# Kernel tuning notes

Hardware: AMD Instinct MI355X
Metric: run time of the kernel (lower is better)

## Reference

```python
import jax, jax.numpy as jnp
import numpy as np

T, B, H = 2048, 8, 16
KF, VF, KS, VS = 32, 64, 128, 64


def _l2norm(x, eps=1e-6):
    return x / jnp.sqrt(jnp.sum(x * x, axis=-1, keepdims=True) + eps)


def setup_inputs() -> dict:
    key = jax.random.key(0)
    ks = jax.random.split(key, 12)
    # k/q are L2-normalized externally (per E88/E90 kernel contract)
    k_fast = _l2norm(jax.random.normal(ks[0], (T, B, H, KF), jnp.float32))
    q_fast = _l2norm(jax.random.normal(ks[1], (T, B, H, KF), jnp.float32))
    v_fast = jax.random.normal(ks[2], (T, B, H, VF), jnp.float32)
    k_slow = _l2norm(jax.random.normal(ks[3], (T, B, H, KS), jnp.float32))
    q_slow = _l2norm(jax.random.normal(ks[4], (T, B, H, KS), jnp.float32))
    v_slow = jax.random.normal(ks[5], (T, B, H, VS), jnp.float32)
    # decay factors in (0.85, 1.0): typical Mamba2-style per-head scalar decay
    decay_fast = 0.85 + 0.15 * jax.random.uniform(ks[6], (T, B, H), jnp.float32)
    decay_slow = 0.85 + 0.15 * jax.random.uniform(ks[7], (T, B, H), jnp.float32)
    slow_gate = jax.random.uniform(ks[8], (T, B, H), jnp.float32)
    mix_fast = jax.random.uniform(ks[9], (T, B, H), jnp.float32)
    mix_slow = jax.random.uniform(ks[10], (T, B, H), jnp.float32)
    S_fast0 = jnp.zeros((B, H, KF, VF), jnp.float32)
    S_slow0 = jnp.zeros((B, H, KS, VS), jnp.float32)
    return dict(k_fast=k_fast, v_fast=v_fast, q_fast=q_fast, decay_fast=decay_fast,
                k_slow=k_slow, v_slow=v_slow, q_slow=q_slow, decay_slow=decay_slow,
                slow_gate=slow_gate, mix_fast=mix_fast, mix_slow=mix_slow,
                S_fast0=S_fast0, S_slow0=S_slow0, n_heads=H)


def _e90_scan(k_fast, v_fast, q_fast, decay_fast,
              k_slow, v_slow, q_slow, decay_slow,
              slow_gate, mix_fast, mix_slow, S_fast0, S_slow0):
    def step(carry, x):
        S_f, S_s = carry  # [B,H,KF,VF], [B,H,KS,VS]
        kf, vf, qf, df, ksl, vsl, qsl, dsl, g, mf, ms = x
        # fast state: updated every timestep (decay + rank-1 outer product)
        S_f = df[..., None, None] * S_f + kf[..., :, None] * vf[..., None, :]
        # slow state: gated soft update
        S_s_new = dsl[..., None, None] * S_s + ksl[..., :, None] * vsl[..., None, :]
        g_ = g[..., None, None]
        S_s = g_ * S_s_new + (1.0 - g_) * S_s
        out_f = jnp.einsum('bhk,bhkv->bhv', qf, S_f)
        out_s = jnp.einsum('bhk,bhkv->bhv', qsl, S_s)
        out = mf[..., None] * out_f + ms[..., None] * out_s
        return (S_f, S_s), out

    xs = (k_fast, v_fast, q_fast, decay_fast,
          k_slow, v_slow, q_slow, decay_slow,
          slow_gate, mix_fast, mix_slow)
    (S_f_final, S_s_final), output = jax.lax.scan(step, (S_fast0, S_slow0), xs)
    return S_f_final, S_s_final, output  # output: [T,B,H,VF]


def reference(k_fast, v_fast, q_fast, decay_fast, k_slow, v_slow, q_slow,
              decay_slow, slow_gate, mix_fast, mix_slow, S_fast0, S_slow0, n_heads):
    return _e90_scan(k_fast, v_fast, q_fast, decay_fast,
                     k_slow, v_slow, q_slow, decay_slow,
                     slow_gate, mix_fast, mix_slow, S_fast0, S_slow0)
```

## Files before the change

### kernel.cpp

```cpp
#include <hip/hip_runtime.h>

#define T_STEPS 2048
#define BH      128
#define KS_     128
#define VS_     64
#define KF_     32
#define VF_     64
#define LCH     32
#define NC      (T_STEPS / LCH)
#define NTHR    512

typedef __attribute__((ext_vector_type(8))) short short8;
typedef __attribute__((ext_vector_type(16))) float f32x16;

#define MFMA32(a,b,c) __builtin_amdgcn_mfma_f32_32x32x16_bf16((a),(b),(c),0,0,0)
#define CROW(r,hi) (((r)&3) + 8*((r)>>2) + 4*(hi))

__device__ __forceinline__ unsigned short f2b(float x) {
    union { float f; unsigned u; } v; v.f = x;
    unsigned r = v.u + 0x7FFFu + ((v.u >> 16) & 1u);
    return (unsigned short)(r >> 16);
}

__device__ __forceinline__ short8 ld8(const unsigned short* p) {
    return *(const short8*)p;
}

__global__ __launch_bounds__(NTHR, 2)
void e90_mfma(const float* __restrict__ k_fast,  const float* __restrict__ v_fast,
              const float* __restrict__ q_fast,  const float* __restrict__ decay_fast,
              const float* __restrict__ k_slow,  const float* __restrict__ v_slow,
              const float* __restrict__ q_slow,  const float* __restrict__ decay_slow,
              const float* __restrict__ slow_gate, const float* __restrict__ mix_fast,
              const float* __restrict__ mix_slow, const float* __restrict__ S_fast0,
              const float* __restrict__ S_slow0, float* __restrict__ dout)
{
    __shared__ __align__(16) unsigned short Qs [LCH][136];
    __shared__ __align__(16) unsigned short Ksl[LCH][136];
    __shared__ __align__(16) unsigned short Sbs[LCH][136];
    __shared__ __align__(16) unsigned short Psl[LCH][40];
    __shared__ __align__(16) unsigned short Qfl[LCH][40];
    __shared__ __align__(16) unsigned short Kfl[LCH][40];
    __shared__ __align__(16) unsigned short Sbfl[LCH][40];
    __shared__ __align__(16) unsigned short Pfl[LCH][40];
    __shared__ __align__(16) unsigned short VTs[2][LCH][40];
    __shared__ __align__(16) unsigned short VTf[2][LCH][40];

    const int tid  = threadIdx.x;
    const int bid  = blockIdx.x;
    const int xcd  = bid & 7;
    const int jj   = bid >> 3;
    const int p    = xcd * 16 + (jj >> 1);
    const int v0   = (jj & 1) * 32;
    const int lane = tid & 63;
    const int wid  = tid >> 6;
    const int l31  = lane & 31;
    const int hi   = lane >> 5;
    const int s_   = tid >> 4;
    const int j0_  = (tid & 15) * 2;
    const int k0_  = (tid & 15) * 8;

    float* out_y = dout + BH*KF_*VF_ + BH*KS_*VS_;

    f32x16 Sst, oacc;
#pragma unroll
    for (int r = 0; r < 16; ++r) { Sst[r] = 0.0f; oacc[r] = 0.0f; }
    if (wid < 4) {
#pragma unroll
        for (int r = 0; r < 16; ++r)
            Sst[r] = S_slow0[((size_t)p*KS_ + 32*wid + CROW(r,hi))*VS_ + v0 + l31];
#pragma unroll
        for (int r = 0; r < 16; ++r) Sbs[l31][32*wid + CROW(r,hi)] = f2b(Sst[r]);
    } else if (wid == 4) {
#pragma unroll
        for (int r = 0; r < 16; ++r)
            Sst[r] = S_fast0[((size_t)p*KF_ + CROW(r,hi))*VF_ + v0 + l31];
#pragma unroll
        for (int r = 0; r < 16; ++r) Sbfl[l31][CROW(r,hi)] = f2b(Sst[r]);
    }

    float4 pKs0, pKs1, pQs0, pQs1;
    float2 pVs, pVf, pKf, pQf;
    float pL0 = 0.f, pL1 = 0.f, pL2 = 0.f;

#define LOADCHUNK(CIDX) do {                                                   \
    int tc_ = (CIDX); if (tc_ > NC-1) tc_ = NC-1;                              \
    const int tb_ = tc_ * LCH;                                                 \
    const float* bk_ = k_slow + ((size_t)(tb_+s_)*BH + p)*KS_ + k0_;           \
    pKs0 = *(const float4*)bk_;  pKs1 = *(const float4*)(bk_+4);               \
    const float* bq_ = q_slow + ((size_t)(tb_+s_)*BH + p)*KS_ + k0_;           \
    pQs0 = *(const float4*)bq_;  pQs1 = *(const float4*)(bq_+4);               \
    pVs = *(const float2*)(v_slow + ((size_t)(tb_+s_)*BH + p)*VS_ + v0 + j0_); \
    pVf = *(const float2*)(v_fast + ((size_t)(tb_+s_)*BH + p)*VF_ + v0 + j0_); \
    pKf = *(const float2*)(k_fast + ((size_t)(tb_+s_)*BH + p)*KF_ + j0_);      \
    pQf = *(const float2*)(q_fast + ((size_t)(tb_+s_)*BH + p)*KF_ + j0_);      \
    const size_t so_ = (size_t)(tb_ + l31)*BH + p;                             \
    pL0 = (hi ? decay_fast : decay_slow)[so_];                                 \
    pL1 = (hi ? mix_fast   : slow_gate )[so_];                                 \
    pL2 = hi ? 0.0f : mix_slow[so_];                                           \
    } while (0)

    LOADCHUNK(0);

    float bls = 1.f, blf = 1.f, ib = 1.f, ibf = 1.f, qsc = 0.f, qfc = 0.f, g_s = 0.f;

    for (int c = 0; c < NC; ++c) {
        const int cb = c & 1;
        if (c > 0) {
            if (wid < 4) {
#pragma unroll
                for (int r = 0; r < 16; ++r) Sbs[l31][32*wid + CROW(r,hi)] = f2b(Sst[r]);
            } else if (wid == 4) {
#pragma unroll
                for (int r = 0; r < 16; ++r) Sbfl[l31][CROW(r,hi)] = f2b(Sst[r]);
            } else if (wid == 7) {
                const int pb = cb ^ 1;
                f32x16 o2;
#pragma unroll
                for (int r = 0; r < 16; ++r) o2[r] = 0.0f;
                const unsigned short* ar = &Psl[l31][0];
                const unsigned short* br = &VTs[pb][l31][0];
                oacc = MFMA32(ld8(ar + 8*hi),      ld8(br + 8*hi),      oacc);
                oacc = MFMA32(ld8(ar + 16 + 8*hi), ld8(br + 16 + 8*hi), oacc);
                const unsigned short* af = &Pfl[l31][0];
                const unsigned short* bf = &VTf[pb][l31][0];
                o2 = MFMA32(ld8(af + 8*hi),      ld8(bf + 8*hi),      o2);
                o2 = MFMA32(ld8(af + 16 + 8*hi), ld8(bf + 16 + 8*hi), o2);
#pragma unroll
                for (int r = 0; r < 16; ++r) {
                    int tr = CROW(r,hi);
                    out_y[((size_t)((c-1)*LCH + tr)*BH + p)*VF_ + v0 + l31] = oacc[r] + o2[r];
                }
            }
        }
        {
            float a = hi ? pL0 : __builtin_fmaf(pL1, pL0, 1.0f - pL1);
            float b = a;
#pragma unroll
            for (int d = 1; d < 32; d <<= 1) {
                float y = __shfl_up(b, d, 32);
                if (l31 >= d) b *= y;
            }
            float bs_s = __shfl(b, s_);
            float bf_s = __shfl(b, 32 + s_);
            bls = __shfl(b, 31);
            blf = __shfl(b, 63);
            g_s = __shfl(pL1, s_);
            float mf_s = __shfl(pL1, 32 + s_);
            float ms_s = __shfl(pL2, s_);
            ib  = 1.0f / bs_s;
            ibf = 1.0f / bf_s;
            qsc = ms_s * bs_s;
            qfc = mf_s * bf_s;
        }
        {
            float kv[8] = {pKs0.x,pKs0.y,pKs0.z,pKs0.w,pKs1.x,pKs1.y,pKs1.z,pKs1.w};
            float qv[8] = {pQs0.x,pQs0.y,pQs0.z,pQs0.w,pQs1.x,pQs1.y,pQs1.z,pQs1.w};
            unsigned short kb[8], qb[8];
#pragma unroll
            for (int e = 0; e < 8; ++e) { kb[e] = f2b(kv[e]*ib); qb[e] = f2b(qv[e]*qsc); }
            uint4 kw, qw;
            kw.x = kb[0] | ((unsigned)kb[1]<<16); kw.y = kb[2] | ((unsigned)kb[3]<<16);
            kw.z = kb[4] | ((unsigned)kb[5]<<16); kw.w = kb[6] | ((unsigned)kb[7]<<16);
            qw.x = qb[0] | ((unsigned)qb[1]<<16); qw.y = qb[2] | ((unsigned)qb[3]<<16);
            qw.z = qb[4] | ((unsigned)qb[5]<<16); qw.w = qb[6] | ((unsigned)qb[7]<<16);
            *(uint4*)&Ksl[s_][k0_] = kw;
            *(uint4*)&Qs [s_][k0_] = qw;

            float vt0 = g_s*pVs.x, vt1 = g_s*pVs.y;
            VTs[cb][j0_  ][s_] = f2b(vt0);
            VTs[cb][j0_+1][s_] = f2b(vt1);
            VTf[cb][j0_  ][s_] = f2b(pVf.x);
            VTf[cb][j0_+1][s_] = f2b(pVf.y);
            unsigned kfp = f2b(pKf.x*ibf) | ((unsigned)f2b(pKf.y*ibf) << 16);
            *(unsigned*)&Kfl[s_][j0_] = kfp;
            unsigned qfp = f2b(pQf.x*qfc) | ((unsigned)f2b(pQf.y*qfc) << 16);
            *(unsigned*)&Qfl[s_][j0_] = qfp;
        }
        __syncthreads();

        LOADCHUNK(c + 1);

        if (wid < 4) {
            short8 a1, a2;
#pragma unroll
            for (int e = 0; e < 8; ++e) {
                a1[e] = (short)Ksl[8*hi + e][32*wid + l31];
                a2[e] = (short)Ksl[16 + 8*hi + e][32*wid + l31];
            }
            const unsigned short* br = &VTs[cb][l31][0];
            Sst = MFMA32(a1, ld8(br + 8*hi),      Sst);
            Sst = MFMA32(a2, ld8(br + 16 + 8*hi), Sst);
#pragma unroll
            for (int r = 0; r < 16; ++r) Sst[r] *= bls;
        } else if (wid == 4) {
            short8 a1, a2;
#pragma unroll
            for (int e = 0; e < 8; ++e) {
                a1[e] = (short)Kfl[8*hi + e][l31];
                a2[e] = (short)Kfl[16 + 8*hi + e][l31];
            }
            const unsigned short* br = &VTf[cb][l31][0];
            Sst = MFMA32(a1, ld8(br + 8*hi),      Sst);
            Sst = MFMA32(a2, ld8(br + 16 + 8*hi), Sst);
#pragma unroll
            for (int r = 0; r < 16; ++r) Sst[r] *= blf;
        } else if (wid == 5) {
            f32x16 p1, p2;
#pragma unroll
            for (int r = 0; r < 16; ++r) { p1[r] = 0.0f; p2[r] = 0.0f; }
            const unsigned short* ar = &Qs [l31][0];
            const unsigned short* br = &Ksl[l31][0];
            const int kb = 8*hi;
#pragma unroll
            for (int st = 0; st < 8; st += 2) {
                p1 = MFMA32(ld8(ar + kb + 16*st),     ld8(br + kb + 16*st),     p1);
                p2 = MFMA32(ld8(ar + kb + 16*(st+1)), ld8(br + kb + 16*(st+1)), p2);
            }
#pragma unroll
            for (int r = 0; r < 16; ++r) {
                int tr = CROW(r,hi);
                Psl[tr][l31] = f2b(tr >= l31 ? p1[r] + p2[r] : 0.0f);
            }
        } else if (wid == 6) {
            f32x16 p1;
#pragma unroll
            for (int r = 0; r < 16; ++r) p1[r] = 0.0f;
            const unsigned short* ar = &Qfl[l31][0];
            const unsigned short* br = &Kfl[l31][0];
            p1 = MFMA32(ld8(ar + 8*hi),      ld8(br + 8*hi),      p1);
            p1 = MFMA32(ld8(ar + 16 + 8*hi), ld8(br + 16 + 8*hi), p1);
#pragma unroll
            for (int r = 0; r < 16; ++r) {
                int tr = CROW(r,hi);
                Pfl[tr][l31] = f2b(tr >= l31 ? p1[r] : 0.0f);
            }
        } else {
            f32x16 o1, o2;
#pragma unroll
            for (int r = 0; r < 16; ++r) { o1[r] = 0.0f; o2[r] = 0.0f; }
            const unsigned short* ar = &Qs [l31][0];
            const unsigned short* br = &Sbs[l31][0];
            const int kb = 8*hi;
#pragma unroll
            for (int st = 0; st < 8; st += 2) {
                o1 = MFMA32(ld8(ar + kb + 16*st),     ld8(br + kb + 16*st),     o1);
                o2 = MFMA32(ld8(ar + kb + 16*(st+1)), ld8(br + kb + 16*(st+1)), o2);
            }
            const unsigned short* af = &Qfl [l31][0];
            const unsigned short* bf = &Sbfl[l31][0];
            o1 = MFMA32(ld8(af + 8*hi),      ld8(bf + 8*hi),      o1);
            o2 = MFMA32(ld8(af + 16 + 8*hi), ld8(bf + 16 + 8*hi), o2);
#pragma unroll
            for (int r = 0; r < 16; ++r) oacc[r] = o1[r] + o2[r];
        }
        __syncthreads();
    }

    if (wid == 7) {
        const int pb = (NC - 1) & 1;
        f32x16 o2;
#pragma unroll
        for (int r = 0; r < 16; ++r) o2[r] = 0.0f;
        const unsigned short* ar = &Psl[l31][0];
        const unsigned short* br = &VTs[pb][l31][0];
        oacc = MFMA32(ld8(ar + 8*hi),      ld8(br + 8*hi),      oacc);
        oacc = MFMA32(ld8(ar + 16 + 8*hi), ld8(br + 16 + 8*hi), oacc);
        const unsigned short* af = &Pfl[l31][0];
        const unsigned short* bf = &VTf[pb][l31][0];
        o2 = MFMA32(ld8(af + 8*hi),      ld8(bf + 8*hi),      o2);
        o2 = MFMA32(ld8(af + 16 + 8*hi), ld8(bf + 16 + 8*hi), o2);
#pragma unroll
        for (int r = 0; r < 16; ++r) {
            int tr = CROW(r,hi);
            out_y[((size_t)((NC-1)*LCH + tr)*BH + p)*VF_ + v0 + l31] = oacc[r] + o2[r];
        }
    }

    if (wid < 4) {
#pragma unroll
        for (int r = 0; r < 16; ++r)
            dout[BH*KF_*VF_ + ((size_t)p*KS_ + 32*wid + CROW(r,hi))*VS_ + v0 + l31] = Sst[r];
    } else if (wid == 4) {
#pragma unroll
        for (int r = 0; r < 16; ++r)
            dout[((size_t)p*KF_ + CROW(r,hi))*VF_ + v0 + l31] = Sst[r];
    }
#undef LOADCHUNK
}

extern "C" void kernel_launch(void* const* d_in, const int* in_sizes, int n_in,
                              void* d_out, int out_size, void* d_ws, size_t ws_size,
                              hipStream_t stream)
{
    const float* k_fast     = (const float*)d_in[0];
    const float* v_fast     = (const float*)d_in[1];
    const float* q_fast     = (const float*)d_in[2];
    const float* decay_fast = (const float*)d_in[3];
    const float* k_slow     = (const float*)d_in[4];
    const float* v_slow     = (const float*)d_in[5];
    const float* q_slow     = (const float*)d_in[6];
    const float* decay_slow = (const float*)d_in[7];
    const float* slow_gate  = (const float*)d_in[8];
    const float* mix_fast   = (const float*)d_in[9];
    const float* mix_slow   = (const float*)d_in[10];
    const float* S_fast0    = (const float*)d_in[11];
    const float* S_slow0    = (const float*)d_in[12];
    float* dout = (float*)d_out;

    e90_mfma<<<dim3(256), dim3(NTHR), 0, stream>>>(
        k_fast, v_fast, q_fast, decay_fast,
        k_slow, v_slow, q_slow, decay_slow,
        slow_gate, mix_fast, mix_slow, S_fast0, S_slow0, dout);
}
```

Baseline: 205.4 us.

## Double-buffer chunk staging to drop a barrier per chunk and use packed bf16 converts

Shared-memory staging buffers are now double-buffered (triple for the V transposes). The next chunk's K/Q/V staging, decay scan and state writeback happen after the current chunk's MFMA work, so each chunk needs one __syncthreads instead of two. The scalar loads are prefetched two chunks ahead. The manual bf16 rounding used for K/Q packing is replaced with the v_cvt_pk_bf16_f32 instruction. This costs more LDS, which could reduce occupancy, and the staging work now sits serially after the compute inside the same barrier interval.

Measured after the change: 186.9 us (median of 2 runs). 9.0% less time.

```diff
diff --git a/kernel.cpp b/kernel.cpp
--- a/kernel.cpp
+++ b/kernel.cpp
@@ -21,7 +21,11 @@
     unsigned r = v.u + 0x7FFFu + ((v.u >> 16) & 1u);
     return (unsigned short)(r >> 16);
 }
-
+__device__ __forceinline__ unsigned cvtpk(float lo, float hi_) {
+    unsigned r;
+    asm("v_cvt_pk_bf16_f32 %0, %1, %2" : "=v"(r) : "v"(lo), "v"(hi_));
+    return r;
+}
 __device__ __forceinline__ short8 ld8(const unsigned short* p) {
     return *(const short8*)p;
 }
@@ -35,16 +39,16 @@
               const float* __restrict__ mix_slow, const float* __restrict__ S_fast0,
               const float* __restrict__ S_slow0, float* __restrict__ dout)
 {
-    __shared__ __align__(16) unsigned short Qs [LCH][136];
-    __shared__ __align__(16) unsigned short Ksl[LCH][136];
-    __shared__ __align__(16) unsigned short Sbs[LCH][136];
-    __shared__ __align__(16) unsigned short Psl[LCH][40];
-    __shared__ __align__(16) unsigned short Qfl[LCH][40];
-    __shared__ __align__(16) unsigned short Kfl[LCH][40];
-    __shared__ __align__(16) unsigned short Sbfl[LCH][40];
-    __shared__ __align__(16) unsigned short Pfl[LCH][40];
-    __shared__ __align__(16) unsigned short VTs[2][LCH][40];
-    __shared__ __align__(16) unsigned short VTf[2][LCH][40];
+    __shared__ __align__(16) unsigned short Qs  [2][LCH][136];
+    __shared__ __align__(16) unsigned short Ksl [2][LCH][136];
+    __shared__ __align__(16) unsigned short Sbs [2][LCH][136];
+    __shared__ __align__(16) unsigned short Psl [2][LCH][40];
+    __shared__ __align__(16) unsigned short Pfl [2][LCH][40];
+    __shared__ __align__(16) unsigned short Qfl [2][LCH][40];
+    __shared__ __align__(16) unsigned short Kfl [2][LCH][40];
+    __shared__ __align__(16) unsigned short Sbfl[2][LCH][40];
+    __shared__ __align__(16) unsigned short VTs [3][LCH][40];
+    __shared__ __align__(16) unsigned short VTf [3][LCH][40];
 
     const int tid  = threadIdx.x;
     const int bid  = blockIdx.x;
@@ -70,20 +74,21 @@
         for (int r = 0; r < 16; ++r)
             Sst[r] = S_slow0[((size_t)p*KS_ + 32*wid + CROW(r,hi))*VS_ + v0 + l31];
 #pragma unroll
-        for (int r = 0; r < 16; ++r) Sbs[l31][32*wid + CROW(r,hi)] = f2b(Sst[r]);
+        for (int r = 0; r < 16; ++r) Sbs[0][l31][32*wid + CROW(r,hi)] = f2b(Sst[r]);
     } else if (wid == 4) {
 #pragma unroll
         for (int r = 0; r < 16; ++r)
             Sst[r] = S_fast0[((size_t)p*KF_ + CROW(r,hi))*VF_ + v0 + l31];
 #pragma unroll
-        for (int r = 0; r < 16; ++r) Sbfl[l31][CROW(r,hi)] = f2b(Sst[r]);
+        for (int r = 0; r < 16; ++r) Sbfl[0][l31][CROW(r,hi)] = f2b(Sst[r]);
     }
 
     float4 pKs0, pKs1, pQs0, pQs1;
     float2 pVs, pVf, pKf, pQf;
     float pL0 = 0.f, pL1 = 0.f, pL2 = 0.f;
-
-#define LOADCHUNK(CIDX) do {                                                   \
+    float bls = 1.f, blf = 1.f, ib = 1.f, ibf = 1.f, qsc = 0.f, qfc = 0.f, g_s = 0.f;
+
+#define LOADVEC(CIDX) do {                                                     \
     int tc_ = (CIDX); if (tc_ > NC-1) tc_ = NC-1;                              \
     const int tb_ = tc_ * LCH;                                                 \
     const float* bk_ = k_slow + ((size_t)(tb_+s_)*BH + p)*KS_ + k0_;           \
@@ -94,101 +99,97 @@
     pVf = *(const float2*)(v_fast + ((size_t)(tb_+s_)*BH + p)*VF_ + v0 + j0_); \
     pKf = *(const float2*)(k_fast + ((size_t)(tb_+s_)*BH + p)*KF_ + j0_);      \
     pQf = *(const float2*)(q_fast + ((size_t)(tb_+s_)*BH + p)*KF_ + j0_);      \
-    const size_t so_ = (size_t)(tb_ + l31)*BH + p;                             \
+    } while (0)
+
+#define LOADSCL(CIDX) do {                                                     \
+    int tc_ = (CIDX); if (tc_ > NC-1) tc_ = NC-1;                              \
+    const size_t so_ = (size_t)(tc_*LCH + l31)*BH + p;                         \
     pL0 = (hi ? decay_fast : decay_slow)[so_];                                 \
     pL1 = (hi ? mix_fast   : slow_gate )[so_];                                 \
     pL2 = hi ? 0.0f : mix_slow[so_];                                           \
     } while (0)
 
-    LOADCHUNK(0);
-
-    float bls = 1.f, blf = 1.f, ib = 1.f, ibf = 1.f, qsc = 0.f, qfc = 0.f, g_s = 0.f;
+#define SCAN() do {                                                            \
+    float a_ = hi ? pL0 : __builtin_fmaf(pL1, pL0, 1.0f - pL1);                \
+    float b_ = a_;                                                             \
+    _Pragma("unroll")                                                          \
+    for (int d = 1; d < 32; d <<= 1) {                                         \
+        float y_ = __shfl_up(b_, d, 32);                                       \
+        if (l31 >= d) b_ *= y_;                                                \
+    }                                                                          \
+    float bs_s = __shfl(b_, s_);                                               \
+    float bf_s = __shfl(b_, 32 + s_);                                          \
+    bls = __shfl(b_, 31);                                                      \
+    blf = __shfl(b_, 63);                                                      \
+    g_s = __shfl(pL1, s_);                                                     \
+    float mf_s = __shfl(pL1, 32 + s_);                                         \
+    float ms_s = __shfl(pL2, s_);                                              \
+    ib  = 1.0f / bs_s;                                                         \
+    ibf = 1.0f / bf_s;                                                         \
+    qsc = ms_s * bs_s;                                                         \
+    qfc = mf_s * bf_s;                                                         \
+    } while (0)
+
+#define STAGE(J2, J3) do {                                                     \
+    uint4 kw, qw;                                                              \
+    kw.x = cvtpk(pKs0.x*ib, pKs0.y*ib);  kw.y = cvtpk(pKs0.z*ib, pKs0.w*ib);   \
+    kw.z = cvtpk(pKs1.x*ib, pKs1.y*ib);  kw.w = cvtpk(pKs1.z*ib, pKs1.w*ib);   \
+    qw.x = cvtpk(pQs0.x*qsc, pQs0.y*qsc); qw.y = cvtpk(pQs0.z*qsc, pQs0.w*qsc);\
+    qw.z = cvtpk(pQs1.x*qsc, pQs1.y*qsc); qw.w = cvtpk(pQs1.z*qsc, pQs1.w*qsc);\
+    *(uint4*)&Ksl[J2][s_][k0_] = kw;                                           \
+    *(uint4*)&Qs [J2][s_][k0_] = qw;                                           \
+    float vt0 = g_s*pVs.x, vt1 = g_s*pVs.y;                                    \
+    VTs[J3][j0_  ][s_] = f2b(vt0);                                             \
+    VTs[J3][j0_+1][s_] = f2b(vt1);                                             \
+    VTf[J3][j0_  ][s_] = f2b(pVf.x);                                           \
+    VTf[J3][j0_+1][s_] = f2b(pVf.y);                                           \
+    unsigned kfp = cvtpk(pKf.x*ibf, pKf.y*ibf);                                \
+    *(unsigned*)&Kfl[J2][s_][j0_] = kfp;                                       \
+    unsigned qfp = cvtpk(pQf.x*qfc, pQf.y*qfc);                                \
+    *(unsigned*)&Qfl[J2][s_][j0_] = qfp;                                       \
+    } while (0)
+
+#define YSTORE(CP) do {                                                        \
+    const int p2_ = (CP) & 1, p3_ = (CP) % 3;                                  \
+    f32x16 o2;                                                                 \
+    _Pragma("unroll")                                                          \
+    for (int r = 0; r < 16; ++r) o2[r] = 0.0f;                                 \
+    const unsigned short* ar = &Psl[p2_][l31][0];                              \
+    const unsigned short* br = &VTs[p3_][l31][0];                              \
+    oacc = MFMA32(ld8(ar + 8*hi),      ld8(br + 8*hi),      oacc);             \
+    oacc = MFMA32(ld8(ar + 16 + 8*hi), ld8(br + 16 + 8*hi), oacc);             \
+    const unsigned short* af = &Pfl[p2_][l31][0];                              \
+    const unsigned short* bf = &VTf[p3_][l31][0];                              \
+    o2 = MFMA32(ld8(af + 8*hi),      ld8(bf + 8*hi),      o2);                 \
+    o2 = MFMA32(ld8(af + 16 + 8*hi), ld8(bf + 16 + 8*hi), o2);                 \
+    _Pragma("unroll")                                                          \
+    for (int r = 0; r < 16; ++r) {                                             \
+        int tr = CROW(r,hi);                                                   \
+        out_y[((size_t)((CP)*LCH + tr)*BH + p)*VF_ + v0 + l31] = oacc[r] + o2[r]; \
+    }                                                                          \
+    } while (0)
+
+    LOADVEC(0);
+    LOADSCL(0);
+    SCAN();
+    LOADSCL(1);
+    STAGE(0, 0);
+    __syncthreads();
 
     for (int c = 0; c < NC; ++c) {
-        const int cb = c & 1;
-        if (c > 0) {
-            if (wid < 4) {
-#pragma unroll
-                for (int r = 0; r < 16; ++r) Sbs[l31][32*wid + CROW(r,hi)] = f2b(Sst[r]);
-            } else if (wid == 4) {
-#pragma unroll
-                for (int r = 0; r < 16; ++r) Sbfl[l31][CROW(r,hi)] = f2b(Sst[r]);
-            } else if (wid == 7) {
-                const int pb = cb ^ 1;
-                f32x16 o2;
-#pragma unroll
-                for (int r = 0; r < 16; ++r) o2[r] = 0.0f;
-                const unsigned short* ar = &Psl[l31][0];
-                const unsigned short* br = &VTs[pb][l31][0];
-                oacc = MFMA32(ld8(ar + 8*hi),      ld8(br + 8*hi),      oacc);
-                oacc = MFMA32(ld8(ar + 16 + 8*hi), ld8(br + 16 + 8*hi), oacc);
-                const unsigned short* af = &Pfl[l31][0];
-                const unsigned short* bf = &VTf[pb][l31][0];
-                o2 = MFMA32(ld8(af + 8*hi),      ld8(bf + 8*hi),      o2);
-                o2 = MFMA32(ld8(af + 16 + 8*hi), ld8(bf + 16 + 8*hi), o2);
-#pragma unroll
-                for (int r = 0; r < 16; ++r) {
-                    int tr = CROW(r,hi);
-                    out_y[((size_t)((c-1)*LCH + tr)*BH + p)*VF_ + v0 + l31] = oacc[r] + o2[r];
-                }
-            }
-        }
-        {
-            float a = hi ? pL0 : __builtin_fmaf(pL1, pL0, 1.0f - pL1);
-            float b = a;
-#pragma unroll
-            for (int d = 1; d < 32; d <<= 1) {
-                float y = __shfl_up(b, d, 32);
-                if (l31 >= d) b *= y;
-            }
-            float bs_s = __shfl(b, s_);
-            float bf_s = __shfl(b, 32 + s_);
-            bls = __shfl(b, 31);
-            blf = __shfl(b, 63);
-            g_s = __shfl(pL1, s_);
-            float mf_s = __shfl(pL1, 32 + s_);
-            float ms_s = __shfl(pL2, s_);
-            ib  = 1.0f / bs_s;
-            ibf = 1.0f / bf_s;
-            qsc = ms_s * bs_s;
-            qfc = mf_s * bf_s;
-        }
-        {
-            float kv[8] = {pKs0.x,pKs0.y,pKs0.z,pKs0.w,pKs1.x,pKs1.y,pKs1.z,pKs1.w};
-            float qv[8] = {pQs0.x,pQs0.y,pQs0.z,pQs0.w,pQs1.x,pQs1.y,pQs1.z,pQs1.w};
-            unsigned short kb[8], qb[8];
-#pragma unroll
-            for (int e = 0; e < 8; ++e) { kb[e] = f2b(kv[e]*ib); qb[e] = f2b(qv[e]*qsc); }
-            uint4 kw, qw;
-            kw.x = kb[0] | ((unsigned)kb[1]<<16); kw.y = kb[2] | ((unsigned)kb[3]<<16);
-            kw.z = kb[4] | ((unsigned)kb[5]<<16); kw.w = kb[6] | ((unsigned)kb[7]<<16);
-            qw.x = qb[0] | ((unsigned)qb[1]<<16); qw.y = qb[2] | ((unsigned)qb[3]<<16);
-            qw.z = qb[4] | ((unsigned)qb[5]<<16); qw.w = qb[6] | ((unsigned)qb[7]<<16);
-            *(uint4*)&Ksl[s_][k0_] = kw;
-            *(uint4*)&Qs [s_][k0_] = qw;
-
-            float vt0 = g_s*pVs.x, vt1 = g_s*pVs.y;
-            VTs[cb][j0_  ][s_] = f2b(vt0);
-            VTs[cb][j0_+1][s_] = f2b(vt1);
-            VTf[cb][j0_  ][s_] = f2b(pVf.x);
-            VTf[cb][j0_+1][s_] = f2b(pVf.y);
-            unsigned kfp = f2b(pKf.x*ibf) | ((unsigned)f2b(pKf.y*ibf) << 16);
-            *(unsigned*)&Kfl[s_][j0_] = kfp;
-            unsigned qfp = f2b(pQf.x*qfc) | ((unsigned)f2b(pQf.y*qfc) << 16);
-            *(unsigned*)&Qfl[s_][j0_] = qfp;
-        }
-        __syncthreads();
-
-        LOADCHUNK(c + 1);
+        const int i2 = c & 1;
+        const int i3 = c % 3;
+
+        LOADVEC(c + 1);
 
         if (wid < 4) {
             short8 a1, a2;
 #pragma unroll
             for (int e = 0; e < 8; ++e) {
-                a1[e] = (short)Ksl[8*hi + e][32*wid + l31];
-                a2[e] = (short)Ksl[16 + 8*hi + e][32*wid + l31];
-            }
-            const unsigned short* br = &VTs[cb][l31][0];
+                a1[e] = (short)Ksl[i2][8*hi + e][32*wid + l31];
+                a2[e] = (short)Ksl[i2][16 + 8*hi + e][32*wid + l31];
+            }
+            const unsigned short* br = &VTs[i3][l31][0];
             Sst = MFMA32(a1, ld8(br + 8*hi),      Sst);
             Sst = MFMA32(a2, ld8(br + 16 + 8*hi), Sst);
 #pragma unroll
@@ -197,10 +198,10 @@
             short8 a1, a2;
 #pragma unroll
             for (int e = 0; e < 8; ++e) {
-                a1[e] = (short)Kfl[8*hi + e][l31];
-                a2[e] = (short)Kfl[16 + 8*hi + e][l31];
-            }
-            const unsigned short* br = &VTf[cb][l31][0];
+                a1[e] = (short)Kfl[i2][8*hi + e][l31];
+                a2[e] = (short)Kfl[i2][16 + 8*hi + e][l31];
+            }
+            const unsigned short* br = &VTf[i3][l31][0];
             Sst = MFMA32(a1, ld8(br + 8*hi),      Sst);
             Sst = MFMA32(a2, ld8(br + 16 + 8*hi), Sst);
 #pragma unroll
@@ -209,8 +210,8 @@
             f32x16 p1, p2;
 #pragma unroll
             for (int r = 0; r < 16; ++r) { p1[r] = 0.0f; p2[r] = 0.0f; }
-            const unsigned short* ar = &Qs [l31][0];
-            const unsigned short* br = &Ksl[l31][0];
+            const unsigned short* ar = &Qs [i2][l31][0];
+            const unsigned short* br = &Ksl[i2][l31][0];
             const int kb = 8*hi;
 #pragma unroll
             for (int st = 0; st < 8; st += 2) {
@@ -220,63 +221,63 @@
 #pragma unroll
             for (int r = 0; r < 16; ++r) {
                 int tr = CROW(r,hi);
-                Psl[tr][l31] = f2b(tr >= l31 ? p1[r] + p2[r] : 0.0f);
+                Psl[i2][tr][l31] = f2b(tr >= l31 ? p1[r] + p2[r] : 0.0f);
             }
         } else if (wid == 6) {
             f32x16 p1;
 #pragma unroll
             for (int r = 0; r < 16; ++r) p1[r] = 0.0f;
-            const unsigned short* ar = &Qfl[l31][0];
-            const unsigned short* br = &Kfl[l31][0];
+            const unsigned short* ar = &Qfl[i2][l31][0];
+            const unsigned short* br = &Kfl[i2][l31][0];
             p1 = MFMA32(ld8(ar + 8*hi),      ld8(br + 8*hi),      p1);
             p1 = MFMA32(ld8(ar + 16 + 8*hi), ld8(br + 16 + 8*hi), p1);
 #pragma unroll
             for (int r = 0; r < 16; ++r) {
                 int tr = CROW(r,hi);
-                Pfl[tr][l31] = f2b(tr >= l31 ? p1[r] : 0.0f);
+                Pfl[i2][tr][l31] = f2b(tr >= l31 ? p1[r] : 0.0f);
             }
         } else {
+            if (c > 0) YSTORE(c - 1);
             f32x16 o1, o2;
 #pragma unroll
             for (int r = 0; r < 16; ++r) { o1[r] = 0.0f; o2[r] = 0.0f; }
-            const unsigned short* ar = &Qs [l31][0];
-            const unsigned short* br = &Sbs[l31][0];
+            const unsigned short* ar = &Qs [i2][l31][0];
+            const unsigned short* br = &Sbs[i2][l31][0];
             const int kb = 8*hi;
 #pragma unroll
             for (int st = 0; st < 8; st += 2) {
                 o1 = MFMA32(ld8(ar + kb + 16*st),     ld8(br + kb + 16*st),     o1);
                 o2 = MFMA32(ld8(ar + kb + 16*(st+1)), ld8(br + kb + 16*(st+1)), o2);
             }
-            const unsigned short* af = &Qfl [l31][0];
-            const unsigned short* bf = &Sbfl[l31][0];
+            const unsigned short* af = &Qfl [i2][l31][0];
+            const unsigned short* bf = &Sbfl[i2][l31][0];
             o1 = MFMA32(ld8(af + 8*hi),      ld8(bf + 8*hi),      o1);
             o2 = MFMA32(ld8(af + 16 + 8*hi), ld8(bf + 16 + 8*hi), o2);
 #pragma unroll
             for (int r = 0; r < 16; ++r) oacc[r] = o1[r] + o2[r];
+        }
+
+        SCAN();
+        LOADSCL(c + 2);
+
+        if (c < NC - 1) {
+            const int j2 = (c + 1) & 1;
+            const int j3 = (c + 1) % 3;
+            if (wid < 4) {
+#pragma unroll
+                for (int r = 0; r < 16; ++r) Sbs[j2][l31][32*wid + CROW(r,hi)] = f2b(Sst[r]);
+            } else if (wid == 4) {
+#pragma unroll
+                for (int r = 0; r < 16; ++r) Sbfl[j2][l31][CROW(r,hi)] = f2b(Sst[r]);
+            }
+            STAGE(j2, j3);
         }
         __syncthreads();
     }
 
     if (wid == 7) {
-        const int pb = (NC - 1) & 1;
-        f32x16 o2;
-#pragma unroll
-        for (int r = 0; r < 16; ++r) o2[r] = 0.0f;
-        const unsigned short* ar = &Psl[l31][0];
-        const unsigned short* br = &VTs[pb][l31][0];
-        oacc = MFMA32(ld8(ar + 8*hi),      ld8(br + 8*hi),      oacc);
-        oacc = MFMA32(ld8(ar + 16 + 8*hi), ld8(br + 16 + 8*hi), oacc);
-        const unsigned short* af = &Pfl[l31][0];
-        const unsigned short* bf = &VTf[pb][l31][0];
-        o2 = MFMA32(ld8(af + 8*hi),      ld8(bf + 8*hi),      o2);
-        o2 = MFMA32(ld8(af + 16 + 8*hi), ld8(bf + 16 + 8*hi), o2);
-#pragma unroll
-        for (int r = 0; r < 16; ++r) {
-            int tr = CROW(r,hi);
-            out_y[((size_t)((NC-1)*LCH + tr)*BH + p)*VF_ + v0 + l31] = oacc[r] + o2[r];
-        }
+        YSTORE(NC - 1);
     }
-
     if (wid < 4) {
 #pragma unroll
         for (int r = 0; r < 16; ++r)
@@ -286,7 +287,11 @@
         for (int r = 0; r < 16; ++r)
             dout[((size_t)p*KF_ + CROW(r,hi))*VF_ + v0 + l31] = Sst[r];
     }
-#undef LOADCHUNK
+#undef LOADVEC
+#undef LOADSCL
+#undef SCAN
+#undef STAGE
+#undef YSTORE
 }
 
 extern "C" void kernel_launch(void* const* d_in, const int* in_sizes, int n_in,
```
